# Optimization experiments

Measured on AMD Instinct MI355X. Metric: run time of the kernel, lower is better.

Reference implementation:

```python
import jax, jax.numpy as jnp
import numpy as np

B, S, D_IN, H, N_NODES, N_EDGES = 32, 1024, 128, 512, 1024, 16384
SPECTRAL = [0.9, 0.8]   # 0.9 - i*0.1
LEAK = [0.1, 0.15]      # 0.1 + i*0.05
INPUT_SCALING, BIAS_SCALING = 1.0, 0.1


def _make_reservoir(rng, h, radius):
    """Random reservoir matrix with 4-population block scaling, normalized to target spectral radius."""
    W = rng.standard_normal((h, h)).astype(np.float64)
    p = h // 4
    bounds = [0, p, 2 * p, 3 * p, h]
    scales = [(1.2, 0.5), (0.8, 1.3), (1.5, 0.7), (1.0, 1.0)]  # (diag_block, off_block)
    for i in range(4):
        s, e = bounds[i], bounds[i + 1]
        diag, off = scales[i]
        diag_block = W[s:e, s:e] * diag
        W[s:e, :] *= off
        W[s:e, s:e] = diag_block
    ev = np.linalg.eigvals(W)
    W *= radius / np.abs(ev).max()
    return W.astype(np.float32)


def _linear(rng, out_f, in_f):
    k = 1.0 / np.sqrt(in_f)
    Wt = rng.uniform(-k, k, (out_f, in_f)).astype(np.float32)
    b = rng.uniform(-k, k, (out_f,)).astype(np.float32)
    return Wt, b


def setup_inputs() -> dict:
    rng = np.random.default_rng(0)
    x = jnp.asarray(rng.standard_normal((B, S, D_IN)).astype(np.float32))
    edge_index = jnp.asarray(rng.integers(0, N_NODES, (2, N_EDGES)), dtype=jnp.int64)
    inp = {"x": x, "edge_index": edge_index}
    in_sizes = [D_IN, H]
    for l in range(2):
        W_in = (rng.standard_normal((H, in_sizes[l])).astype(np.float32) * INPUT_SCALING)
        W_res = _make_reservoir(rng, H, SPECTRAL[l])
        bias = (rng.standard_normal((H,)).astype(np.float32) * BIAS_SCALING)
        Wp, bp = _linear(rng, N_NODES, H)   # graph_proj: hidden -> num_nodes
        Wu, bu = _linear(rng, H, N_NODES)   # graph_unproj: num_nodes -> hidden
        inp.update({f"W_in{l}": jnp.asarray(W_in), f"W_res{l}": jnp.asarray(W_res),
                    f"bias{l}": jnp.asarray(bias), f"Wp{l}": jnp.asarray(Wp),
                    f"bp{l}": jnp.asarray(bp), f"Wu{l}": jnp.asarray(Wu),
                    f"bu{l}": jnp.asarray(bu)})
    return inp


def _run_layer(x, W_in, W_res, bias, Wp, bp, Wu, bu, src, dst, leak):
    # x: (B, S, D); recurrent scan over time.
    def step(h, x_t):
        inp = x_t @ W_in.T                      # (B, H)
        res = h @ W_res.T                       # (B, H)
        hg = h @ Wp.T + bp                      # (B, N) project onto graph nodes
        # scatter-add message passing: aggr[b, dst] += hg[b, src]
        aggr = jnp.zeros_like(hg).at[:, dst].add(hg[:, src])
        gc = aggr @ Wu.T + bu                   # (B, H)
        h_new = jnp.tanh(inp + res + gc + bias)
        h = (1.0 - leak) * h + leak * h_new     # leaky integration
        return h, h
    h0 = jnp.zeros((x.shape[0], W_res.shape[0]), x.dtype)
    _, ys = jax.lax.scan(step, h0, jnp.swapaxes(x, 0, 1))  # ys: (S, B, H)
    return jnp.swapaxes(ys, 0, 1)


def reference(x, edge_index,
              W_in0, W_res0, bias0, Wp0, bp0, Wu0, bu0,
              W_in1, W_res1, bias1, Wp1, bp1, Wu1, bu1):
    src, dst = edge_index[0], edge_index[1]
    h = _run_layer(x, W_in0, W_res0, bias0, Wp0, bp0, Wu0, bu0, src, dst, LEAK[0])
    h = _run_layer(h, W_in1, W_res1, bias1, Wp1, bp1, Wu1, bu1, src, dst, LEAK[1])
    return h  # dropout is identity in eval mode
```

## Files before the change

### kernel.cpp

```cpp
#include <hip/hip_runtime.h>
#include <hip/hip_bf16.h>
#include <cstddef>
#include <cstdint>

#define HDIM 512
#define NNODES 1024
#define NEDGES 16384
#define BATCH 32
#define SEQ 1024
#define DIN 128
#define SLICES 8

#define RLX __ATOMIC_RELAXED
#define AGT __HIP_MEMORY_SCOPE_AGENT

__global__ void scatter_awp_kernel(const float* __restrict__ Wp,
                                   const int* __restrict__ src,
                                   const int* __restrict__ dst,
                                   float* __restrict__ AWp) {
    int e = blockIdx.x;
    int c = threadIdx.x;
    int s = src[e], d = dst[e];
    atomicAdd(&AWp[d * HDIM + c],       Wp[s * HDIM + c]);
    atomicAdd(&AWp[d * HDIM + 256 + c], Wp[s * HDIM + 256 + c]);
}

__global__ void scatter_abp_kernel(const float* __restrict__ bp,
                                   const int* __restrict__ src,
                                   const int* __restrict__ dst,
                                   float* __restrict__ Abp) {
    int e = blockIdx.x * blockDim.x + threadIdx.x;
    if (e < NEDGES) atomicAdd(&Abp[dst[e]], bp[src[e]]);
}

__global__ void beff_kernel(const float* __restrict__ Wu,
                            const float* __restrict__ Abp,
                            const float* __restrict__ bias,
                            const float* __restrict__ bu,
                            float* __restrict__ beff) {
    int i = threadIdx.x;
    float s = 0.f;
    for (int d = 0; d < NNODES; ++d) s += Wu[i * NNODES + d] * Abp[d];
    beff[i] = bias[i] + bu[i] + s;
}

template <int TB>
__global__ __launch_bounds__(256) void gemm64(const float* __restrict__ A,
                                              const float* __restrict__ B,
                                              float* __restrict__ C,
                                              const float* __restrict__ addend,
                                              int M, int N, int K) {
    const int bn = blockIdx.x, bm = blockIdx.y;
    const int tid = threadIdx.x;
    const int tx = tid & 15, ty = tid >> 4;
    const int m0 = bm * 64, n0 = bn * 64;

    __shared__ float As[16][68];
    __shared__ float Bs[16][68];

    float acc[4][4] = {};

    for (int k0 = 0; k0 < K; k0 += 16) {
        {
            int kk = tid & 15, m = tid >> 4;
            #pragma unroll
            for (int i = 0; i < 4; ++i)
                As[kk][m + 16 * i] = A[(size_t)(m0 + m + 16 * i) * K + k0 + kk];
        }
        if (TB == 0) {
            int n = tid & 63, kk = tid >> 6;
            #pragma unroll
            for (int i = 0; i < 4; ++i)
                Bs[kk + 4 * i][n] = B[(size_t)(k0 + kk + 4 * i) * N + n0 + n];
        } else {
            int kk = tid & 15, n = tid >> 4;
            #pragma unroll
            for (int i = 0; i < 4; ++i)
                Bs[kk][n + 16 * i] = B[(size_t)(n0 + n + 16 * i) * K + k0 + kk];
        }
        __syncthreads();
        #pragma unroll
        for (int kk = 0; kk < 16; ++kk) {
            float4 a4 = *reinterpret_cast<const float4*>(&As[kk][ty * 4]);
            float4 b4 = *reinterpret_cast<const float4*>(&Bs[kk][tx * 4]);
            float av[4] = {a4.x, a4.y, a4.z, a4.w};
            float bv[4] = {b4.x, b4.y, b4.z, b4.w};
            #pragma unroll
            for (int i = 0; i < 4; ++i)
                #pragma unroll
                for (int j = 0; j < 4; ++j)
                    acc[i][j] += av[i] * bv[j];
        }
        __syncthreads();
    }
    #pragma unroll
    for (int i = 0; i < 4; ++i) {
        int m = m0 + ty * 4 + i;
        #pragma unroll
        for (int j = 0; j < 4; ++j) {
            int n = n0 + tx * 4 + j;
            float v = acc[i][j];
            if (addend) v += addend[(size_t)m * N + n];
            C[(size_t)m * N + n] = v;
        }
    }
}

template <int CTRL, int RMASK, bool BC>
__device__ __forceinline__ float dpp_add(float x) {
    int t = __builtin_amdgcn_update_dpp(0, __float_as_int(x), CTRL, RMASK, 0xf, BC);
    return x + __int_as_float(t);
}

__device__ __forceinline__ float reduce32(float x) {
    x = dpp_add<0x111, 0xf, true>(x);
    x = dpp_add<0x112, 0xf, true>(x);
    x = dpp_add<0x114, 0xf, true>(x);
    x = dpp_add<0x118, 0xf, true>(x);
    x = dpp_add<0x142, 0xa, false>(x);
    return x;
}

__device__ __forceinline__ float fast_tanh(float x) {
    float e = __expf(2.0f * x);
    return 1.0f - 2.0f / (e + 1.0f);
}

__launch_bounds__(512, 1)
__global__ void scan2_kernel(const float* __restrict__ Weff0,
                             const float* __restrict__ beff0,
                             const float* __restrict__ Weff1,
                             const float* __restrict__ beff1,
                             const float* __restrict__ Win1,
                             const float* __restrict__ u0,
                             float* __restrict__ out,
                             unsigned long long* __restrict__ hp0,
                             unsigned long long* __restrict__ hp1) {
    const int slice = blockIdx.x;
    const int b = blockIdx.y;
    const int tid = threadIdx.x;
    const int c = tid & 31;
    const int hw = tid >> 5;
    const int rloc = hw * 4;
    const int rowbase = slice * 64 + rloc;
    const bool storer = (c == 31);
    const size_t SLOTS = (size_t)BATCH * HDIM;

    __shared__ float wl0[64 * HDIM];
    __shared__ float hs0[2][HDIM];
    __shared__ float hs1[2][HDIM];

    {
        const float4* src4 = reinterpret_cast<const float4*>(
            Weff0 + (size_t)slice * 64 * HDIM);
        float4* dst4 = reinterpret_cast<float4*>(wl0);
        #pragma unroll
        for (int i = 0; i < 16; ++i)
            dst4[tid + 512 * i] = src4[tid + 512 * i];
    }

    float4 be04 = make_float4(0.f, 0.f, 0.f, 0.f);
    float4 be14 = make_float4(0.f, 0.f, 0.f, 0.f);
    if (storer) {
        be04 = *reinterpret_cast<const float4*>(beff0 + rowbase);
        be14 = *reinterpret_cast<const float4*>(beff1 + rowbase);
    }
    const float lk0 = 0.10f, olk0 = 0.90f;
    const float lk1 = 0.15f, olk1 = 0.85f;
    const float* u0b = u0 + (size_t)b * SEQ * HDIM;
    float* ob = out + (size_t)b * SEQ * HDIM;
    unsigned long long* h0b = hp0 + (size_t)b * HDIM;
    unsigned long long* h1b = hp1 + (size_t)b * HDIM;
    float4 hold0 = make_float4(0.f, 0.f, 0.f, 0.f);
    float4 hold1 = make_float4(0.f, 0.f, 0.f, 0.f);

    __syncthreads();

    for (int i = 0; i <= SEQ; ++i) {
        float4 wq[4][4], wi[4][4];
        #pragma unroll
        for (int r = 0; r < 4; ++r)
            #pragma unroll
            for (int k = 0; k < 4; ++k) {
                const int co = 4 * (c + 32 * k);
                wq[r][k] = *reinterpret_cast<const float4*>(
                    Weff1 + (size_t)(rowbase + r) * HDIM + co);
                wi[r][k] = *reinterpret_cast<const float4*>(
                    Win1 + (size_t)(rowbase + r) * HDIM + co);
            }
        float4 u4 = make_float4(0.f, 0.f, 0.f, 0.f);
        if (storer && i < SEQ)
            u4 = *reinterpret_cast<const float4*>(u0b + (size_t)i * HDIM + rowbase);

        const unsigned long long* sp0 = h0b + (size_t)(i & 1) * SLOTS + tid;
        const unsigned long long* sp1 = h1b + (size_t)((i - 1) & 1) * SLOTS + tid;

        unsigned long long v1 = 0ull;
        if (i >= 1) v1 = __hip_atomic_load(sp1, RLX, AGT);

        unsigned long long v0 = __hip_atomic_load(sp0, RLX, AGT);
        while ((unsigned)(v0 >> 32) != (unsigned)i)
            v0 = __hip_atomic_load(sp0, RLX, AGT);
        hs0[i & 1][tid] = __uint_as_float((unsigned)v0);
        __syncthreads();

        if (i < SEQ) {
            float a0 = 0.f, a1 = 0.f, a2 = 0.f, a3 = 0.f;
            const float* h = hs0[i & 1];
            #pragma unroll
            for (int k = 0; k < 4; ++k) {
                const int co = 4 * (c + 32 * k);
                float4 h4 = *reinterpret_cast<const float4*>(h + co);
                float4 w0 = *reinterpret_cast<const float4*>(&wl0[(rloc + 0) * HDIM + co]);
                float4 w1 = *reinterpret_cast<const float4*>(&wl0[(rloc + 1) * HDIM + co]);
                float4 w2 = *reinterpret_cast<const float4*>(&wl0[(rloc + 2) * HDIM + co]);
                float4 w3 = *reinterpret_cast<const float4*>(&wl0[(rloc + 3) * HDIM + co]);
                a0 += w0.x * h4.x + w0.y * h4.y + w0.z * h4.z + w0.w * h4.w;
                a1 += w1.x * h4.x + w1.y * h4.y + w1.z * h4.z + w1.w * h4.w;
                a2 += w2.x * h4.x + w2.y * h4.y + w2.z * h4.z + w2.w * h4.w;
                a3 += w3.x * h4.x + w3.y * h4.y + w3.z * h4.z + w3.w * h4.w;
            }
            a0 = reduce32(a0);
            a1 = reduce32(a1);
            a2 = reduce32(a2);
            a3 = reduce32(a3);
            if (storer) {
                float n0 = olk0 * hold0.x + lk0 * fast_tanh(a0 + u4.x + be04.x);
                float n1 = olk0 * hold0.y + lk0 * fast_tanh(a1 + u4.y + be04.y);
                float n2 = olk0 * hold0.z + lk0 * fast_tanh(a2 + u4.z + be04.z);
                float n3 = olk0 * hold0.w + lk0 * fast_tanh(a3 + u4.w + be04.w);
                hold0 = make_float4(n0, n1, n2, n3);
                unsigned long long tg = ((unsigned long long)(unsigned)(i + 1)) << 32;
                unsigned long long* hp = h0b + (size_t)((i + 1) & 1) * SLOTS + rowbase;
                __hip_atomic_store(hp + 0, tg | __float_as_uint(n0), RLX, AGT);
                __hip_atomic_store(hp + 1, tg | __float_as_uint(n1), RLX, AGT);
                __hip_atomic_store(hp + 2, tg | __float_as_uint(n2), RLX, AGT);
                __hip_atomic_store(hp + 3, tg | __float_as_uint(n3), RLX, AGT);
            }
        }

        if (i >= 1) {
            while ((unsigned)(v1 >> 32) != (unsigned)(i - 1))
                v1 = __hip_atomic_load(sp1, RLX, AGT);
            hs1[(i - 1) & 1][tid] = __uint_as_float((unsigned)v1);
        }
        __syncthreads();

        if (i >= 1) {
            float g0 = 0.f, g1 = 0.f, g2 = 0.f, g3 = 0.f;
            const float* h0v = hs0[i & 1];
            const float* h1v = hs1[(i - 1) & 1];
            #pragma unroll
            for (int k = 0; k < 4; ++k) {
                const int co = 4 * (c + 32 * k);
                float4 p4 = *reinterpret_cast<const float4*>(h0v + co);
                float4 q4 = *reinterpret_cast<const float4*>(h1v + co);
                g0 += wi[0][k].x * p4.x + wi[0][k].y * p4.y + wi[0][k].z * p4.z + wi[0][k].w * p4.w
                    + wq[0][k].x * q4.x + wq[0][k].y * q4.y + wq[0][k].z * q4.z + wq[0][k].w * q4.w;
                g1 += wi[1][k].x * p4.x + wi[1][k].y * p4.y + wi[1][k].z * p4.z + wi[1][k].w * p4.w
                    + wq[1][k].x * q4.x + wq[1][k].y * q4.y + wq[1][k].z * q4.z + wq[1][k].w * q4.w;
                g2 += wi[2][k].x * p4.x + wi[2][k].y * p4.y + wi[2][k].z * p4.z + wi[2][k].w * p4.w
                    + wq[2][k].x * q4.x + wq[2][k].y * q4.y + wq[2][k].z * q4.z + wq[2][k].w * q4.w;
                g3 += wi[3][k].x * p4.x + wi[3][k].y * p4.y + wi[3][k].z * p4.z + wi[3][k].w * p4.w
                    + wq[3][k].x * q4.x + wq[3][k].y * q4.y + wq[3][k].z * q4.z + wq[3][k].w * q4.w;
            }
            g0 = reduce32(g0);
            g1 = reduce32(g1);
            g2 = reduce32(g2);
            g3 = reduce32(g3);
            if (storer) {
                float m0 = olk1 * hold1.x + lk1 * fast_tanh(g0 + be14.x);
                float m1 = olk1 * hold1.y + lk1 * fast_tanh(g1 + be14.y);
                float m2 = olk1 * hold1.z + lk1 * fast_tanh(g2 + be14.z);
                float m3 = olk1 * hold1.w + lk1 * fast_tanh(g3 + be14.w);
                hold1 = make_float4(m0, m1, m2, m3);
                unsigned long long tg = ((unsigned long long)(unsigned)i) << 32;
                unsigned long long* hp = h1b + (size_t)(i & 1) * SLOTS + rowbase;
                __hip_atomic_store(hp + 0, tg | __float_as_uint(m0), RLX, AGT);
                __hip_atomic_store(hp + 1, tg | __float_as_uint(m1), RLX, AGT);
                __hip_atomic_store(hp + 2, tg | __float_as_uint(m2), RLX, AGT);
                __hip_atomic_store(hp + 3, tg | __float_as_uint(m3), RLX, AGT);
                *reinterpret_cast<float4*>(ob + (size_t)(i - 1) * HDIM + rowbase) =
                    make_float4(m0, m1, m2, m3);
            }
        }
    }
}

extern "C" void kernel_launch(void* const* d_in, const int* in_sizes, int n_in,
                              void* d_out, int out_size, void* d_ws, size_t ws_size,
                              hipStream_t stream) {
    const float* x      = (const float*)d_in[0];
    const int*   edges  = (const int*)d_in[1];
    const float* W_in0  = (const float*)d_in[2];
    const float* W_res0 = (const float*)d_in[3];
    const float* bias0  = (const float*)d_in[4];
    const float* Wp0    = (const float*)d_in[5];
    const float* bp0    = (const float*)d_in[6];
    const float* Wu0    = (const float*)d_in[7];
    const float* bu0    = (const float*)d_in[8];
    const float* W_in1  = (const float*)d_in[9];
    const float* W_res1 = (const float*)d_in[10];
    const float* bias1  = (const float*)d_in[11];
    const float* Wp1    = (const float*)d_in[12];
    const float* bp1    = (const float*)d_in[13];
    const float* Wu1    = (const float*)d_in[14];
    const float* bu1    = (const float*)d_in[15];

    const int* src = edges;
    const int* dst = edges + NEDGES;
    float* out = (float*)d_out;

    char* base = (char*)d_ws;
    float* ws_u  = (float*)base;
    char* p = base + (size_t)67108864;
    float* AWp   = (float*)p;  p += 2097152;
    float* Abp   = (float*)p;  p += 4096;
    float* Weff0 = (float*)p;  p += 1048576;
    float* Weff1 = (float*)p;  p += 1048576;
    float* beff0 = (float*)p;  p += 2048;
    float* beff1 = (float*)p;  p += 2048;
    unsigned long long* hp0 = (unsigned long long*)p;  p += 262144;
    unsigned long long* hp1 = (unsigned long long*)p;  p += 262144;

    hipMemsetAsync(AWp, 0, 2097152 + 4096, stream);
    scatter_awp_kernel<<<NEDGES, 256, 0, stream>>>(Wp0, src, dst, AWp);
    scatter_abp_kernel<<<NEDGES / 256, 256, 0, stream>>>(bp0, src, dst, Abp);
    gemm64<0><<<dim3(8, 8), 256, 0, stream>>>(Wu0, AWp, Weff0, W_res0, 512, 512, 1024);
    beff_kernel<<<1, 512, 0, stream>>>(Wu0, Abp, bias0, bu0, beff0);

    hipMemsetAsync(AWp, 0, 2097152 + 4096, stream);
    scatter_awp_kernel<<<NEDGES, 256, 0, stream>>>(Wp1, src, dst, AWp);
    scatter_abp_kernel<<<NEDGES / 256, 256, 0, stream>>>(bp1, src, dst, Abp);
    gemm64<0><<<dim3(8, 8), 256, 0, stream>>>(Wu1, AWp, Weff1, W_res1, 512, 512, 1024);
    beff_kernel<<<1, 512, 0, stream>>>(Wu1, Abp, bias1, bu1, beff1);

    gemm64<1><<<dim3(512 / 64, 32768 / 64), 256, 0, stream>>>(
        x, W_in0, ws_u, nullptr, BATCH * SEQ, HDIM, DIN);

    hipMemsetAsync(hp0, 0, 524288, stream);
    scan2_kernel<<<dim3(SLICES, BATCH), 512, 0, stream>>>(
        Weff0, beff0, Weff1, beff1, W_in1, ws_u, out, hp0, hp1);
}
```

Baseline: 3.501 ms.

## Split two-layer scan into separate layer blocks with ring buffer and fp16 weights

The fused two-layer recurrent scan becomes two groups of blocks, one per layer. Layer 0 runs ahead of layer 1 through an 8-deep ring of tagged hidden states, with a progress counter providing back-pressure. Recurrent weights are held in LDS as fp16 so both layers fit, and W_in1 is pre-converted to fp16 to halve its per-step global reads. This lets the layers pipeline instead of sharing one critical path, at the cost of fp16 weight precision and twice as many co-resident blocks spinning on atomics.

After: 4.075 ms. +16.4%, slower.

```diff
diff --git a/kernel.cpp b/kernel.cpp
--- a/kernel.cpp
+++ b/kernel.cpp
@@ -1,5 +1,6 @@
 #include <hip/hip_runtime.h>
 #include <hip/hip_bf16.h>
+#include <hip/hip_fp16.h>
 #include <cstddef>
 #include <cstdint>
 
@@ -9,7 +10,7 @@
 #define BATCH 32
 #define SEQ 1024
 #define DIN 128
-#define SLICES 8
+#define RING 8
 
 #define RLX __ATOMIC_RELAXED
 #define AGT __HIP_MEMORY_SCOPE_AGENT
@@ -42,6 +43,12 @@
     float s = 0.f;
     for (int d = 0; d < NNODES; ++d) s += Wu[i * NNODES + d] * Abp[d];
     beff[i] = bias[i] + bu[i] + s;
+}
+
+__global__ void tof16_kernel(const float* __restrict__ in,
+                             __half* __restrict__ out, int n) {
+    int i = blockIdx.x * blockDim.x + threadIdx.x;
+    if (i < n) out[i] = __float2half_rn(in[i]);
 }
 
 template <int TB>
@@ -126,16 +133,17 @@
     return 1.0f - 2.0f / (e + 1.0f);
 }
 
-__launch_bounds__(512, 1)
-__global__ void scan2_kernel(const float* __restrict__ Weff0,
-                             const float* __restrict__ beff0,
-                             const float* __restrict__ Weff1,
-                             const float* __restrict__ beff1,
-                             const float* __restrict__ Win1,
-                             const float* __restrict__ u0,
-                             float* __restrict__ out,
-                             unsigned long long* __restrict__ hp0,
-                             unsigned long long* __restrict__ hp1) {
+__launch_bounds__(512, 4)
+__global__ void scan_split_kernel(const float* __restrict__ Weff0,
+                                  const float* __restrict__ beff0,
+                                  const float* __restrict__ Weff1,
+                                  const float* __restrict__ beff1,
+                                  const __half* __restrict__ Win1h,
+                                  const float* __restrict__ u0,
+                                  float* __restrict__ out,
+                                  unsigned long long* __restrict__ hp0,
+                                  unsigned long long* __restrict__ hp1,
+                                  unsigned* __restrict__ prog1) {
     const int slice = blockIdx.x;
     const int b = blockIdx.y;
     const int tid = threadIdx.x;
@@ -146,141 +154,179 @@
     const bool storer = (c == 31);
     const size_t SLOTS = (size_t)BATCH * HDIM;
 
-    __shared__ float wl0[64 * HDIM];
-    __shared__ float hs0[2][HDIM];
-    __shared__ float hs1[2][HDIM];
-
-    {
-        const float4* src4 = reinterpret_cast<const float4*>(
-            Weff0 + (size_t)slice * 64 * HDIM);
-        float4* dst4 = reinterpret_cast<float4*>(wl0);
-        #pragma unroll
-        for (int i = 0; i < 16; ++i)
-            dst4[tid + 512 * i] = src4[tid + 512 * i];
-    }
-
-    float4 be04 = make_float4(0.f, 0.f, 0.f, 0.f);
-    float4 be14 = make_float4(0.f, 0.f, 0.f, 0.f);
-    if (storer) {
-        be04 = *reinterpret_cast<const float4*>(beff0 + rowbase);
-        be14 = *reinterpret_cast<const float4*>(beff1 + rowbase);
-    }
-    const float lk0 = 0.10f, olk0 = 0.90f;
-    const float lk1 = 0.15f, olk1 = 0.85f;
-    const float* u0b = u0 + (size_t)b * SEQ * HDIM;
-    float* ob = out + (size_t)b * SEQ * HDIM;
-    unsigned long long* h0b = hp0 + (size_t)b * HDIM;
-    unsigned long long* h1b = hp1 + (size_t)b * HDIM;
-    float4 hold0 = make_float4(0.f, 0.f, 0.f, 0.f);
-    float4 hold1 = make_float4(0.f, 0.f, 0.f, 0.f);
-
-    __syncthreads();
-
-    for (int i = 0; i <= SEQ; ++i) {
-        float4 wq[4][4], wi[4][4];
-        #pragma unroll
-        for (int r = 0; r < 4; ++r)
+    __shared__ __align__(16) unsigned char smembuf[73728];
+
+    if (blockIdx.z == 0) {
+        __half* wl = (__half*)smembuf;
+        float (*hs)[HDIM] = (float(*)[HDIM])(smembuf + 65536);
+
+        {
+            const float4* src4 = reinterpret_cast<const float4*>(
+                Weff0 + (size_t)slice * 64 * HDIM);
+            __half2* dst2 = reinterpret_cast<__half2*>(wl);
+            #pragma unroll
+            for (int i = 0; i < 16; ++i) {
+                float4 v = src4[tid + 512 * i];
+                dst2[2 * (tid + 512 * i)]     = __floats2half2_rn(v.x, v.y);
+                dst2[2 * (tid + 512 * i) + 1] = __floats2half2_rn(v.z, v.w);
+            }
+        }
+        float4 be4 = make_float4(0.f, 0.f, 0.f, 0.f);
+        if (storer) be4 = *reinterpret_cast<const float4*>(beff0 + rowbase);
+        const float lk = 0.10f, olk = 0.90f;
+        const float* ub = u0 + (size_t)b * SEQ * HDIM;
+        float4 hold = make_float4(0.f, 0.f, 0.f, 0.f);
+        __syncthreads();
+
+        for (int i = 0; i < SEQ; ++i) {
+            float4 u4 = make_float4(0.f, 0.f, 0.f, 0.f);
+            if (storer)
+                u4 = *reinterpret_cast<const float4*>(ub + (size_t)i * HDIM + rowbase);
+
+            if (i >= RING && tid < 8) {
+                while ((int)__hip_atomic_load(&prog1[b * 8 + tid], RLX, AGT) < i - (RING - 1)) {}
+            }
+
+            const unsigned long long* sp = hp0 + (size_t)(i & (RING - 1)) * SLOTS
+                                         + (size_t)b * HDIM + tid;
+            unsigned long long v = __hip_atomic_load(sp, RLX, AGT);
+            while ((unsigned)(v >> 32) != (unsigned)i)
+                v = __hip_atomic_load(sp, RLX, AGT);
+            hs[i & 1][tid] = __uint_as_float((unsigned)v);
+            __syncthreads();
+
+            float a0 = 0.f, a1 = 0.f, a2 = 0.f, a3 = 0.f;
+            const float* hv = hs[i & 1];
             #pragma unroll
             for (int k = 0; k < 4; ++k) {
                 const int co = 4 * (c + 32 * k);
-                wq[r][k] = *reinterpret_cast<const float4*>(
-                    Weff1 + (size_t)(rowbase + r) * HDIM + co);
-                wi[r][k] = *reinterpret_cast<const float4*>(
-                    Win1 + (size_t)(rowbase + r) * HDIM + co);
-            }
-        float4 u4 = make_float4(0.f, 0.f, 0.f, 0.f);
-        if (storer && i < SEQ)
-            u4 = *reinterpret_cast<const float4*>(u0b + (size_t)i * HDIM + rowbase);
-
-        const unsigned long long* sp0 = h0b + (size_t)(i & 1) * SLOTS + tid;
-        const unsigned long long* sp1 = h1b + (size_t)((i - 1) & 1) * SLOTS + tid;
-
-        unsigned long long v1 = 0ull;
-        if (i >= 1) v1 = __hip_atomic_load(sp1, RLX, AGT);
-
-        unsigned long long v0 = __hip_atomic_load(sp0, RLX, AGT);
-        while ((unsigned)(v0 >> 32) != (unsigned)i)
-            v0 = __hip_atomic_load(sp0, RLX, AGT);
-        hs0[i & 1][tid] = __uint_as_float((unsigned)v0);
-        __syncthreads();
-
-        if (i < SEQ) {
-            float a0 = 0.f, a1 = 0.f, a2 = 0.f, a3 = 0.f;
-            const float* h = hs0[i & 1];
-            #pragma unroll
-            for (int k = 0; k < 4; ++k) {
-                const int co = 4 * (c + 32 * k);
-                float4 h4 = *reinterpret_cast<const float4*>(h + co);
-                float4 w0 = *reinterpret_cast<const float4*>(&wl0[(rloc + 0) * HDIM + co]);
-                float4 w1 = *reinterpret_cast<const float4*>(&wl0[(rloc + 1) * HDIM + co]);
-                float4 w2 = *reinterpret_cast<const float4*>(&wl0[(rloc + 2) * HDIM + co]);
-                float4 w3 = *reinterpret_cast<const float4*>(&wl0[(rloc + 3) * HDIM + co]);
-                a0 += w0.x * h4.x + w0.y * h4.y + w0.z * h4.z + w0.w * h4.w;
-                a1 += w1.x * h4.x + w1.y * h4.y + w1.z * h4.z + w1.w * h4.w;
-                a2 += w2.x * h4.x + w2.y * h4.y + w2.z * h4.z + w2.w * h4.w;
-                a3 += w3.x * h4.x + w3.y * h4.y + w3.z * h4.z + w3.w * h4.w;
+                float4 h4 = *reinterpret_cast<const float4*>(hv + co);
+                #pragma unroll
+                for (int r = 0; r < 4; ++r) {
+                    __half2 p = *reinterpret_cast<const __half2*>(&wl[(rloc + r) * HDIM + co]);
+                    __half2 q = *reinterpret_cast<const __half2*>(&wl[(rloc + r) * HDIM + co + 2]);
+                    float2 pf = __half22float2(p);
+                    float2 qf = __half22float2(q);
+                    float acc = pf.x * h4.x + pf.y * h4.y + qf.x * h4.z + qf.y * h4.w;
+                    if (r == 0) a0 += acc;
+                    else if (r == 1) a1 += acc;
+                    else if (r == 2) a2 += acc;
+                    else a3 += acc;
+                }
             }
             a0 = reduce32(a0);
             a1 = reduce32(a1);
             a2 = reduce32(a2);
             a3 = reduce32(a3);
+
             if (storer) {
-                float n0 = olk0 * hold0.x + lk0 * fast_tanh(a0 + u4.x + be04.x);
-                float n1 = olk0 * hold0.y + lk0 * fast_tanh(a1 + u4.y + be04.y);
-                float n2 = olk0 * hold0.z + lk0 * fast_tanh(a2 + u4.z + be04.z);
-                float n3 = olk0 * hold0.w + lk0 * fast_tanh(a3 + u4.w + be04.w);
-                hold0 = make_float4(n0, n1, n2, n3);
+                float n0 = olk * hold.x + lk * fast_tanh(a0 + u4.x + be4.x);
+                float n1 = olk * hold.y + lk * fast_tanh(a1 + u4.y + be4.y);
+                float n2 = olk * hold.z + lk * fast_tanh(a2 + u4.z + be4.z);
+                float n3 = olk * hold.w + lk * fast_tanh(a3 + u4.w + be4.w);
+                hold = make_float4(n0, n1, n2, n3);
                 unsigned long long tg = ((unsigned long long)(unsigned)(i + 1)) << 32;
-                unsigned long long* hp = h0b + (size_t)((i + 1) & 1) * SLOTS + rowbase;
+                unsigned long long* hp = hp0 + (size_t)((i + 1) & (RING - 1)) * SLOTS
+                                       + (size_t)b * HDIM + rowbase;
                 __hip_atomic_store(hp + 0, tg | __float_as_uint(n0), RLX, AGT);
                 __hip_atomic_store(hp + 1, tg | __float_as_uint(n1), RLX, AGT);
                 __hip_atomic_store(hp + 2, tg | __float_as_uint(n2), RLX, AGT);
                 __hip_atomic_store(hp + 3, tg | __float_as_uint(n3), RLX, AGT);
             }
         }
-
-        if (i >= 1) {
-            while ((unsigned)(v1 >> 32) != (unsigned)(i - 1))
+    } else {
+        __half* wl1 = (__half*)smembuf;
+        float (*hs0)[HDIM] = (float(*)[HDIM])(smembuf + 65536);
+        float (*hs1)[HDIM] = (float(*)[HDIM])(smembuf + 69632);
+
+        {
+            const float4* src4 = reinterpret_cast<const float4*>(
+                Weff1 + (size_t)slice * 64 * HDIM);
+            __half2* dst2 = reinterpret_cast<__half2*>(wl1);
+            #pragma unroll
+            for (int i = 0; i < 16; ++i) {
+                float4 v = src4[tid + 512 * i];
+                dst2[2 * (tid + 512 * i)]     = __floats2half2_rn(v.x, v.y);
+                dst2[2 * (tid + 512 * i) + 1] = __floats2half2_rn(v.z, v.w);
+            }
+        }
+        float4 be4 = make_float4(0.f, 0.f, 0.f, 0.f);
+        if (storer) be4 = *reinterpret_cast<const float4*>(beff1 + rowbase);
+        const float lk = 0.15f, olk = 0.85f;
+        float* ob = out + (size_t)b * SEQ * HDIM;
+        float4 hold = make_float4(0.f, 0.f, 0.f, 0.f);
+        __syncthreads();
+
+        for (int j = 1; j <= SEQ; ++j) {
+            uint2 wi16[4][4];
+            #pragma unroll
+            for (int r = 0; r < 4; ++r)
+                #pragma unroll
+                for (int k = 0; k < 4; ++k) {
+                    const int co = 4 * (c + 32 * k);
+                    wi16[r][k] = *reinterpret_cast<const uint2*>(
+                        Win1h + (size_t)(rowbase + r) * HDIM + co);
+                }
+
+            const unsigned long long* sp1 = hp1 + (size_t)((j - 1) & 1) * SLOTS
+                                          + (size_t)b * HDIM + tid;
+            unsigned long long v1 = __hip_atomic_load(sp1, RLX, AGT);
+            const unsigned long long* sp0 = hp0 + (size_t)(j & (RING - 1)) * SLOTS
+                                          + (size_t)b * HDIM + tid;
+            unsigned long long v0 = __hip_atomic_load(sp0, RLX, AGT);
+            while ((unsigned)(v0 >> 32) != (unsigned)j)
+                v0 = __hip_atomic_load(sp0, RLX, AGT);
+            hs0[j & 1][tid] = __uint_as_float((unsigned)v0);
+            while ((unsigned)(v1 >> 32) != (unsigned)(j - 1))
                 v1 = __hip_atomic_load(sp1, RLX, AGT);
-            hs1[(i - 1) & 1][tid] = __uint_as_float((unsigned)v1);
-        }
-        __syncthreads();
-
-        if (i >= 1) {
+            hs1[(j - 1) & 1][tid] = __uint_as_float((unsigned)v1);
+            __syncthreads();
+            if (tid == 0)
+                __hip_atomic_store(&prog1[b * 8 + slice], (unsigned)j, RLX, AGT);
+
             float g0 = 0.f, g1 = 0.f, g2 = 0.f, g3 = 0.f;
-            const float* h0v = hs0[i & 1];
-            const float* h1v = hs1[(i - 1) & 1];
+            const float* h0v = hs0[j & 1];
+            const float* h1v = hs1[(j - 1) & 1];
             #pragma unroll
             for (int k = 0; k < 4; ++k) {
                 const int co = 4 * (c + 32 * k);
                 float4 p4 = *reinterpret_cast<const float4*>(h0v + co);
                 float4 q4 = *reinterpret_cast<const float4*>(h1v + co);
-                g0 += wi[0][k].x * p4.x + wi[0][k].y * p4.y + wi[0][k].z * p4.z + wi[0][k].w * p4.w
-                    + wq[0][k].x * q4.x + wq[0][k].y * q4.y + wq[0][k].z * q4.z + wq[0][k].w * q4.w;
-                g1 += wi[1][k].x * p4.x + wi[1][k].y * p4.y + wi[1][k].z * p4.z + wi[1][k].w * p4.w
-                    + wq[1][k].x * q4.x + wq[1][k].y * q4.y + wq[1][k].z * q4.z + wq[1][k].w * q4.w;
-                g2 += wi[2][k].x * p4.x + wi[2][k].y * p4.y + wi[2][k].z * p4.z + wi[2][k].w * p4.w
-                    + wq[2][k].x * q4.x + wq[2][k].y * q4.y + wq[2][k].z * q4.z + wq[2][k].w * q4.w;
-                g3 += wi[3][k].x * p4.x + wi[3][k].y * p4.y + wi[3][k].z * p4.z + wi[3][k].w * p4.w
-                    + wq[3][k].x * q4.x + wq[3][k].y * q4.y + wq[3][k].z * q4.z + wq[3][k].w * q4.w;
+                #pragma unroll
+                for (int r = 0; r < 4; ++r) {
+                    float2 wa = __half22float2(*reinterpret_cast<const __half2*>(&wi16[r][k].x));
+                    float2 wb = __half22float2(*reinterpret_cast<const __half2*>(&wi16[r][k].y));
+                    __half2 ea = *reinterpret_cast<const __half2*>(&wl1[(rloc + r) * HDIM + co]);
+                    __half2 eb = *reinterpret_cast<const __half2*>(&wl1[(rloc + r) * HDIM + co + 2]);
+                    float2 ef = __half22float2(ea);
+                    float2 eg = __half22float2(eb);
+                    float acc = wa.x * p4.x + wa.y * p4.y + wb.x * p4.z + wb.y * p4.w
+                              + ef.x * q4.x + ef.y * q4.y + eg.x * q4.z + eg.y * q4.w;
+                    if (r == 0) g0 += acc;
+                    else if (r == 1) g1 += acc;
+                    else if (r == 2) g2 += acc;
+                    else g3 += acc;
+                }
             }
             g0 = reduce32(g0);
             g1 = reduce32(g1);
             g2 = reduce32(g2);
             g3 = reduce32(g3);
+
             if (storer) {
-                float m0 = olk1 * hold1.x + lk1 * fast_tanh(g0 + be14.x);
-                float m1 = olk1 * hold1.y + lk1 * fast_tanh(g1 + be14.y);
-                float m2 = olk1 * hold1.z + lk1 * fast_tanh(g2 + be14.z);
-                float m3 = olk1 * hold1.w + lk1 * fast_tanh(g3 + be14.w);
-                hold1 = make_float4(m0, m1, m2, m3);
-                unsigned long long tg = ((unsigned long long)(unsigned)i) << 32;
-                unsigned long long* hp = h1b + (size_t)(i & 1) * SLOTS + rowbase;
+                float m0 = olk * hold.x + lk * fast_tanh(g0 + be4.x);
+                float m1 = olk * hold.y + lk * fast_tanh(g1 + be4.y);
+                float m2 = olk * hold.z + lk * fast_tanh(g2 + be4.z);
+                float m3 = olk * hold.w + lk * fast_tanh(g3 + be4.w);
+                hold = make_float4(m0, m1, m2, m3);
+                unsigned long long tg = ((unsigned long long)(unsigned)j) << 32;
+                unsigned long long* hp = hp1 + (size_t)(j & 1) * SLOTS
+                                       + (size_t)b * HDIM + rowbase;
                 __hip_atomic_store(hp + 0, tg | __float_as_uint(m0), RLX, AGT);
                 __hip_atomic_store(hp + 1, tg | __float_as_uint(m1), RLX, AGT);
                 __hip_atomic_store(hp + 2, tg | __float_as_uint(m2), RLX, AGT);
                 __hip_atomic_store(hp + 3, tg | __float_as_uint(m3), RLX, AGT);
-                *reinterpret_cast<float4*>(ob + (size_t)(i - 1) * HDIM + rowbase) =
+                *reinterpret_cast<float4*>(ob + (size_t)(j - 1) * HDIM + rowbase) =
                     make_float4(m0, m1, m2, m3);
             }
         }
@@ -312,24 +358,29 @@
     float* out = (float*)d_out;
 
     char* base = (char*)d_ws;
-    float* ws_u  = (float*)base;
-    char* p = base + (size_t)67108864;
-    float* AWp   = (float*)p;  p += 2097152;
-    float* Abp   = (float*)p;  p += 4096;
-    float* Weff0 = (float*)p;  p += 1048576;
-    float* Weff1 = (float*)p;  p += 1048576;
-    float* beff0 = (float*)p;  p += 2048;
-    float* beff1 = (float*)p;  p += 2048;
-    unsigned long long* hp0 = (unsigned long long*)p;  p += 262144;
-    unsigned long long* hp1 = (unsigned long long*)p;  p += 262144;
-
-    hipMemsetAsync(AWp, 0, 2097152 + 4096, stream);
+    float* ws_u = (float*)base;
+    char* q = base + (size_t)67108864;
+    float* AWp = (float*)q;
+    unsigned long long* hp0 = (unsigned long long*)q;
+    unsigned long long* hp1 = (unsigned long long*)(q + 1048576);
+    unsigned* prog1 = (unsigned*)(q + 1310720);
+    __half* Win1h = (__half*)(q + 1314816);
+    char* p2 = q + 2097152;
+    float* Abp   = (float*)p2;
+    float* Weff0 = (float*)(p2 + 4096);
+    float* Weff1 = (float*)(p2 + 1052672);
+    float* beff0 = (float*)(p2 + 2101248);
+    float* beff1 = (float*)(p2 + 2103296);
+
+    hipMemsetAsync(AWp, 0, 2097152, stream);
+    hipMemsetAsync(Abp, 0, 4096, stream);
     scatter_awp_kernel<<<NEDGES, 256, 0, stream>>>(Wp0, src, dst, AWp);
     scatter_abp_kernel<<<NEDGES / 256, 256, 0, stream>>>(bp0, src, dst, Abp);
     gemm64<0><<<dim3(8, 8), 256, 0, stream>>>(Wu0, AWp, Weff0, W_res0, 512, 512, 1024);
     beff_kernel<<<1, 512, 0, stream>>>(Wu0, Abp, bias0, bu0, beff0);
 
-    hipMemsetAsync(AWp, 0, 2097152 + 4096, stream);
+    hipMemsetAsync(AWp, 0, 2097152, stream);
+    hipMemsetAsync(Abp, 0, 4096, stream);
     scatter_awp_kernel<<<NEDGES, 256, 0, stream>>>(Wp1, src, dst, AWp);
     scatter_abp_kernel<<<NEDGES / 256, 256, 0, stream>>>(bp1, src, dst, Abp);
     gemm64<0><<<dim3(8, 8), 256, 0, stream>>>(Wu1, AWp, Weff1, W_res1, 512, 512, 1024);
@@ -338,7 +389,9 @@
     gemm64<1><<<dim3(512 / 64, 32768 / 64), 256, 0, stream>>>(
         x, W_in0, ws_u, nullptr, BATCH * SEQ, HDIM, DIN);
 
-    hipMemsetAsync(hp0, 0, 524288, stream);
-    scan2_kernel<<<dim3(SLICES, BATCH), 512, 0, stream>>>(
-        Weff0, beff0, Weff1, beff1, W_in1, ws_u, out, hp0, hp1);
-}
+    hipMemsetAsync(q, 0, 1314816 + 4096, stream);
+    tof16_kernel<<<HDIM * HDIM / 1024, 1024, 0, stream>>>(W_in1, Win1h, HDIM * HDIM);
+
+    scan_split_kernel<<<dim3(8, BATCH, 2), 512, 0, stream>>>(
+        Weff0, beff0, Weff1, beff1, Win1h, ws_u, out, hp0, hp1, prog1);
+}
```

## Convert scan weights and hidden states to fp16 and use fdot2 accumulation

Applied to the files above, without the earlier changes.

The recurrent scan kernel now keeps both effective recurrent weight slices (layer 0 and layer 1) in LDS as fp16. It broadcasts the hidden state as fp16 and accumulates in fp32 via v_dot2 instructions. Weff1 is no longer re-read from global memory every step, and W_in1 is pre-converted to fp16 to halve its per-step global traffic. Workspace buffers are reused to hold the fp16 copy. The cost is reduced precision of weights and hidden state inside a 1024-step recurrence, which risks accumulating error.

Result: no change. 3.448 ms (-1.5%).

```diff
diff --git a/kernel.cpp b/kernel.cpp
--- a/kernel.cpp
+++ b/kernel.cpp
@@ -1,5 +1,6 @@
 #include <hip/hip_runtime.h>
 #include <hip/hip_bf16.h>
+#include <hip/hip_fp16.h>
 #include <cstddef>
 #include <cstdint>
 
@@ -13,6 +14,8 @@
 
 #define RLX __ATOMIC_RELAXED
 #define AGT __HIP_MEMORY_SCOPE_AGENT
+
+typedef _Float16 h2 __attribute__((ext_vector_type(2)));
 
 __global__ void scatter_awp_kernel(const float* __restrict__ Wp,
                                    const int* __restrict__ src,
@@ -42,6 +45,12 @@
     float s = 0.f;
     for (int d = 0; d < NNODES; ++d) s += Wu[i * NNODES + d] * Abp[d];
     beff[i] = bias[i] + bu[i] + s;
+}
+
+__global__ void tof16_kernel(const float* __restrict__ in,
+                             __half* __restrict__ out, int n) {
+    int i = blockIdx.x * blockDim.x + threadIdx.x;
+    if (i < n) out[i] = __float2half_rn(in[i]);
 }
 
 template <int TB>
@@ -126,12 +135,20 @@
     return 1.0f - 2.0f / (e + 1.0f);
 }
 
+__device__ __forceinline__ float fdot2(h2 a, h2 b, float c) {
+#if __has_builtin(__builtin_amdgcn_fdot2)
+    return __builtin_amdgcn_fdot2(a, b, c, false);
+#else
+    return c + (float)a.x * (float)b.x + (float)a.y * (float)b.y;
+#endif
+}
+
 __launch_bounds__(512, 1)
 __global__ void scan2_kernel(const float* __restrict__ Weff0,
                              const float* __restrict__ beff0,
                              const float* __restrict__ Weff1,
                              const float* __restrict__ beff1,
-                             const float* __restrict__ Win1,
+                             const __half* __restrict__ Win1h,
                              const float* __restrict__ u0,
                              float* __restrict__ out,
                              unsigned long long* __restrict__ hp0,
@@ -146,17 +163,30 @@
     const bool storer = (c == 31);
     const size_t SLOTS = (size_t)BATCH * HDIM;
 
-    __shared__ float wl0[64 * HDIM];
-    __shared__ float hs0[2][HDIM];
-    __shared__ float hs1[2][HDIM];
+    __shared__ __align__(16) __half wl0[64 * HDIM];
+    __shared__ __align__(16) __half wl1[64 * HDIM];
+    __shared__ __align__(16) __half hs0[2][HDIM];
+    __shared__ __align__(16) __half hs1[2][HDIM];
 
     {
-        const float4* src4 = reinterpret_cast<const float4*>(
+        const float4* s0 = reinterpret_cast<const float4*>(
             Weff0 + (size_t)slice * 64 * HDIM);
-        float4* dst4 = reinterpret_cast<float4*>(wl0);
+        const float4* s1 = reinterpret_cast<const float4*>(
+            Weff1 + (size_t)slice * 64 * HDIM);
+        h2* d0 = reinterpret_cast<h2*>(wl0);
+        h2* d1 = reinterpret_cast<h2*>(wl1);
         #pragma unroll
-        for (int i = 0; i < 16; ++i)
-            dst4[tid + 512 * i] = src4[tid + 512 * i];
+        for (int i = 0; i < 16; ++i) {
+            const int idx = tid + 512 * i;
+            float4 v = s0[idx];
+            h2 a = {(_Float16)v.x, (_Float16)v.y};
+            h2 bb = {(_Float16)v.z, (_Float16)v.w};
+            d0[2 * idx] = a;  d0[2 * idx + 1] = bb;
+            float4 w = s1[idx];
+            h2 e = {(_Float16)w.x, (_Float16)w.y};
+            h2 f = {(_Float16)w.z, (_Float16)w.w};
+            d1[2 * idx] = e;  d1[2 * idx + 1] = f;
+        }
     }
 
     float4 be04 = make_float4(0.f, 0.f, 0.f, 0.f);
@@ -177,17 +207,18 @@
     __syncthreads();
 
     for (int i = 0; i <= SEQ; ++i) {
-        float4 wq[4][4], wi[4][4];
+        h2 wi[4][4][2];
         #pragma unroll
-        for (int r = 0; r < 4; ++r)
+        for (int r = 0; r < 4; ++r) {
+            const h2* wp = reinterpret_cast<const h2*>(
+                Win1h + (size_t)(rowbase + r) * HDIM);
             #pragma unroll
             for (int k = 0; k < 4; ++k) {
-                const int co = 4 * (c + 32 * k);
-                wq[r][k] = *reinterpret_cast<const float4*>(
-                    Weff1 + (size_t)(rowbase + r) * HDIM + co);
-                wi[r][k] = *reinterpret_cast<const float4*>(
-                    Win1 + (size_t)(rowbase + r) * HDIM + co);
-            }
+                const int cq = 2 * (c + 32 * k);
+                wi[r][k][0] = wp[cq];
+                wi[r][k][1] = wp[cq + 1];
+            }
+        }
         float4 u4 = make_float4(0.f, 0.f, 0.f, 0.f);
         if (storer && i < SEQ)
             u4 = *reinterpret_cast<const float4*>(u0b + (size_t)i * HDIM + rowbase);
@@ -201,24 +232,24 @@
         unsigned long long v0 = __hip_atomic_load(sp0, RLX, AGT);
         while ((unsigned)(v0 >> 32) != (unsigned)i)
             v0 = __hip_atomic_load(sp0, RLX, AGT);
-        hs0[i & 1][tid] = __uint_as_float((unsigned)v0);
+        hs0[i & 1][tid] = __float2half(__uint_as_float((unsigned)v0));
         __syncthreads();
 
         if (i < SEQ) {
             float a0 = 0.f, a1 = 0.f, a2 = 0.f, a3 = 0.f;
-            const float* h = hs0[i & 1];
+            const h2* hv = reinterpret_cast<const h2*>(&hs0[i & 1][0]);
             #pragma unroll
             for (int k = 0; k < 4; ++k) {
-                const int co = 4 * (c + 32 * k);
-                float4 h4 = *reinterpret_cast<const float4*>(h + co);
-                float4 w0 = *reinterpret_cast<const float4*>(&wl0[(rloc + 0) * HDIM + co]);
-                float4 w1 = *reinterpret_cast<const float4*>(&wl0[(rloc + 1) * HDIM + co]);
-                float4 w2 = *reinterpret_cast<const float4*>(&wl0[(rloc + 2) * HDIM + co]);
-                float4 w3 = *reinterpret_cast<const float4*>(&wl0[(rloc + 3) * HDIM + co]);
-                a0 += w0.x * h4.x + w0.y * h4.y + w0.z * h4.z + w0.w * h4.w;
-                a1 += w1.x * h4.x + w1.y * h4.y + w1.z * h4.z + w1.w * h4.w;
-                a2 += w2.x * h4.x + w2.y * h4.y + w2.z * h4.z + w2.w * h4.w;
-                a3 += w3.x * h4.x + w3.y * h4.y + w3.z * h4.z + w3.w * h4.w;
+                const int cq = 2 * (c + 32 * k);
+                h2 ha = hv[cq], hb = hv[cq + 1];
+                const h2* w0 = reinterpret_cast<const h2*>(wl0) + (rloc + 0) * 256 + cq;
+                const h2* w1 = reinterpret_cast<const h2*>(wl0) + (rloc + 1) * 256 + cq;
+                const h2* w2 = reinterpret_cast<const h2*>(wl0) + (rloc + 2) * 256 + cq;
+                const h2* w3 = reinterpret_cast<const h2*>(wl0) + (rloc + 3) * 256 + cq;
+                a0 = fdot2(w0[0], ha, a0); a0 = fdot2(w0[1], hb, a0);
+                a1 = fdot2(w1[0], ha, a1); a1 = fdot2(w1[1], hb, a1);
+                a2 = fdot2(w2[0], ha, a2); a2 = fdot2(w2[1], hb, a2);
+                a3 = fdot2(w3[0], ha, a3); a3 = fdot2(w3[1], hb, a3);
             }
             a0 = reduce32(a0);
             a1 = reduce32(a1);
@@ -242,27 +273,31 @@
         if (i >= 1) {
             while ((unsigned)(v1 >> 32) != (unsigned)(i - 1))
                 v1 = __hip_atomic_load(sp1, RLX, AGT);
-            hs1[(i - 1) & 1][tid] = __uint_as_float((unsigned)v1);
+            hs1[(i - 1) & 1][tid] = __float2half(__uint_as_float((unsigned)v1));
         }
         __syncthreads();
 
         if (i >= 1) {
             float g0 = 0.f, g1 = 0.f, g2 = 0.f, g3 = 0.f;
-            const float* h0v = hs0[i & 1];
-            const float* h1v = hs1[(i - 1) & 1];
+            const h2* pv = reinterpret_cast<const h2*>(&hs0[i & 1][0]);
+            const h2* qv = reinterpret_cast<const h2*>(&hs1[(i - 1) & 1][0]);
             #pragma unroll
             for (int k = 0; k < 4; ++k) {
-                const int co = 4 * (c + 32 * k);
-                float4 p4 = *reinterpret_cast<const float4*>(h0v + co);
-                float4 q4 = *reinterpret_cast<const float4*>(h1v + co);
-                g0 += wi[0][k].x * p4.x + wi[0][k].y * p4.y + wi[0][k].z * p4.z + wi[0][k].w * p4.w
-                    + wq[0][k].x * q4.x + wq[0][k].y * q4.y + wq[0][k].z * q4.z + wq[0][k].w * q4.w;
-                g1 += wi[1][k].x * p4.x + wi[1][k].y * p4.y + wi[1][k].z * p4.z + wi[1][k].w * p4.w
-                    + wq[1][k].x * q4.x + wq[1][k].y * q4.y + wq[1][k].z * q4.z + wq[1][k].w * q4.w;
-                g2 += wi[2][k].x * p4.x + wi[2][k].y * p4.y + wi[2][k].z * p4.z + wi[2][k].w * p4.w
-                    + wq[2][k].x * q4.x + wq[2][k].y * q4.y + wq[2][k].z * q4.z + wq[2][k].w * q4.w;
-                g3 += wi[3][k].x * p4.x + wi[3][k].y * p4.y + wi[3][k].z * p4.z + wi[3][k].w * p4.w
-                    + wq[3][k].x * q4.x + wq[3][k].y * q4.y + wq[3][k].z * q4.z + wq[3][k].w * q4.w;
+                const int cq = 2 * (c + 32 * k);
+                h2 pa = pv[cq], pb = pv[cq + 1];
+                h2 qa = qv[cq], qb = qv[cq + 1];
+                const h2* e0 = reinterpret_cast<const h2*>(wl1) + (rloc + 0) * 256 + cq;
+                const h2* e1 = reinterpret_cast<const h2*>(wl1) + (rloc + 1) * 256 + cq;
+                const h2* e2 = reinterpret_cast<const h2*>(wl1) + (rloc + 2) * 256 + cq;
+                const h2* e3 = reinterpret_cast<const h2*>(wl1) + (rloc + 3) * 256 + cq;
+                g0 = fdot2(wi[0][k][0], pa, g0); g0 = fdot2(wi[0][k][1], pb, g0);
+                g0 = fdot2(e0[0], qa, g0);       g0 = fdot2(e0[1], qb, g0);
+                g1 = fdot2(wi[1][k][0], pa, g1); g1 = fdot2(wi[1][k][1], pb, g1);
+                g1 = fdot2(e1[0], qa, g1);       g1 = fdot2(e1[1], qb, g1);
+                g2 = fdot2(wi[2][k][0], pa, g2); g2 = fdot2(wi[2][k][1], pb, g2);
+                g2 = fdot2(e2[0], qa, g2);       g2 = fdot2(e2[1], qb, g2);
+                g3 = fdot2(wi[3][k][0], pa, g3); g3 = fdot2(wi[3][k][1], pb, g3);
+                g3 = fdot2(e3[0], qa, g3);       g3 = fdot2(e3[1], qb, g3);
             }
             g0 = reduce32(g0);
             g1 = reduce32(g1);
@@ -312,24 +347,28 @@
     float* out = (float*)d_out;
 
     char* base = (char*)d_ws;
-    float* ws_u  = (float*)base;
-    char* p = base + (size_t)67108864;
-    float* AWp   = (float*)p;  p += 2097152;
-    float* Abp   = (float*)p;  p += 4096;
-    float* Weff0 = (float*)p;  p += 1048576;
-    float* Weff1 = (float*)p;  p += 1048576;
-    float* beff0 = (float*)p;  p += 2048;
-    float* beff1 = (float*)p;  p += 2048;
-    unsigned long long* hp0 = (unsigned long long*)p;  p += 262144;
-    unsigned long long* hp1 = (unsigned long long*)p;  p += 262144;
-
-    hipMemsetAsync(AWp, 0, 2097152 + 4096, stream);
+    float* ws_u = (float*)base;
+    char* q = base + (size_t)67108864;
+    float* AWp = (float*)q;
+    unsigned long long* hp0 = (unsigned long long*)q;
+    unsigned long long* hp1 = (unsigned long long*)(q + 262144);
+    __half* Win1h = (__half*)(q + 524288);
+    char* p2 = q + 2097152;
+    float* Abp   = (float*)p2;
+    float* Weff0 = (float*)(p2 + 4096);
+    float* Weff1 = (float*)(p2 + 1052672);
+    float* beff0 = (float*)(p2 + 2101248);
+    float* beff1 = (float*)(p2 + 2103296);
+
+    hipMemsetAsync(AWp, 0, 2097152, stream);
+    hipMemsetAsync(Abp, 0, 4096, stream);
     scatter_awp_kernel<<<NEDGES, 256, 0, stream>>>(Wp0, src, dst, AWp);
     scatter_abp_kernel<<<NEDGES / 256, 256, 0, stream>>>(bp0, src, dst, Abp);
     gemm64<0><<<dim3(8, 8), 256, 0, stream>>>(Wu0, AWp, Weff0, W_res0, 512, 512, 1024);
     beff_kernel<<<1, 512, 0, stream>>>(Wu0, Abp, bias0, bu0, beff0);
 
-    hipMemsetAsync(AWp, 0, 2097152 + 4096, stream);
+    hipMemsetAsync(AWp, 0, 2097152, stream);
+    hipMemsetAsync(Abp, 0, 4096, stream);
     scatter_awp_kernel<<<NEDGES, 256, 0, stream>>>(Wp1, src, dst, AWp);
     scatter_abp_kernel<<<NEDGES / 256, 256, 0, stream>>>(bp1, src, dst, Abp);
     gemm64<0><<<dim3(8, 8), 256, 0, stream>>>(Wu1, AWp, Weff1, W_res1, 512, 512, 1024);
@@ -338,7 +377,9 @@
     gemm64<1><<<dim3(512 / 64, 32768 / 64), 256, 0, stream>>>(
         x, W_in0, ws_u, nullptr, BATCH * SEQ, HDIM, DIN);
 
-    hipMemsetAsync(hp0, 0, 524288, stream);
+    hipMemsetAsync(q, 0, 524288, stream);
+    tof16_kernel<<<HDIM * HDIM / 1024, 1024, 0, stream>>>(W_in1, Win1h, HDIM * HDIM);
+
     scan2_kernel<<<dim3(SLICES, BATCH), 512, 0, stream>>>(
-        Weff0, beff0, Weff1, beff1, W_in1, ws_u, out, hp0, hp1);
-}
+        Weff0, beff0, Weff1, beff1, Win1h, ws_u, out, hp0, hp1);
+}
```
